# Optimization experiments

Hardware: AMD Instinct MI355X
Metric: run time of the kernel (lower is better)

The kernel has to match this reference:

```python
import jax, jax.numpy as jnp
import numpy as np

W_RAD = 2  # box-filter radius (init kwarg w)
KSIZE = 2 * W_RAD + 1


def _box_conv3d(x, kernel):
    # x: [B,1,D,H,W], kernel: [1,1,k,k,k]; 'same' padding, stride 1
    return jax.lax.conv_general_dilated(
        x, kernel,
        window_strides=(1, 1, 1),
        padding=[(W_RAD, W_RAD)] * 3,
        dimension_numbers=("NCDHW", "OIDHW", "NCDHW"),
    )


def setup_inputs() -> dict:
    key = jax.random.key(0)
    k1, k2 = jax.random.split(key)
    shape = (2, 1, 160, 160, 160)
    M = jax.random.uniform(k1, shape, dtype=jnp.float32)
    R = jax.random.uniform(k2, shape, dtype=jnp.float32)
    kernel = jnp.ones((1, 1, KSIZE, KSIZE, KSIZE), dtype=jnp.float32) / (KSIZE ** 3)
    return {"M": M, "R": R, "kernel": kernel}


def reference(M, R, kernel):
    M_m = _box_conv3d(M, kernel)
    R_m = _box_conv3d(R, kernel)
    MM_m = _box_conv3d(M * M, kernel)
    RR_m = _box_conv3d(R * R, kernel)
    MR_m = _box_conv3d(M * R, kernel)
    M_var = jnp.sqrt(MM_m - M_m ** 2 + 1e-05)
    R_var = jnp.sqrt(RR_m - R_m ** 2 + 1e-05)
    corr = (MR_m - M_m * R_m) / (M_var * R_var + 1e-05)
    return -jnp.mean(corr)
```

## Files before the change

kernel.cpp:

```cpp
#include <hip/hip_runtime.h>
#include <math.h>

#define Dd 160
#define Hh 160
#define Ww 160
#define TW 32
#define TH 32
#define DCHUNK 16
#define NSLICE (DCHUNK + 4)
#define NT 320
#define NCH 5
#define PDIM 36
#define SLICE (Hh * Ww)
#define NDC (Dd / DCHUNK)

__global__ void lncc_zero(float* out) { out[0] = 0.0f; }

__device__ __forceinline__ void bar_lgkm() {
    asm volatile("s_waitcnt lgkmcnt(0)" ::: "memory");
    __builtin_amdgcn_s_barrier();
    asm volatile("" ::: "memory");
}

__global__ __launch_bounds__(NT, 2)
void lncc_main(const float* __restrict__ M, const float* __restrict__ R,
               const float* __restrict__ kern, float* __restrict__ out)
{
    __shared__ float sw[2][NCH][TW][PDIM];
    __shared__ float red[NT / 64];

    const int tid = threadIdx.x;
    const int w0 = blockIdx.x * TW;
    const int h0 = blockIdx.y * TH;
    const int b  = blockIdx.z / NDC;
    const int d0 = (blockIdx.z % NDC) * DCHUNK;
    const float k0 = kern[0];

    const bool isB = tid < (TH + 4) * 8;
    const int g   = tid & 7;
    const int row = tid >> 3;
    const int gh  = h0 + row - 2;
    const bool hok = isB && gh >= 0 && gh < Hh;
    bool qok[3]; int qoff[3];
#pragma unroll
    for (int k = 0; k < 3; ++k) {
        int gw = w0 - 4 + 4 * (g + k);
        qok[k]  = hok && gw >= 0 && gw <= Ww - 4;
        qoff[k] = gh * Ww + gw;
    }
    const size_t bb = (size_t)b * Dd * SLICE;
    const float* Mb = M + bb;
    const float* Rb = R + bb;

    float4 cm[2][3], cr[2][3];

    auto issue = [&](int s, int pp) {
        int dd = d0 - 2 + s;
        bool dok = dd >= 0 && dd < Dd;
        const float* Ms = Mb + (size_t)(dok ? dd : 0) * SLICE;
        const float* Rs = Rb + (size_t)(dok ? dd : 0) * SLICE;
#pragma unroll
        for (int k = 0; k < 3; ++k) {
            bool ok = dok && qok[k];
            cm[pp][k] = ok ? *(const float4*)(Ms + qoff[k]) : make_float4(0.f, 0.f, 0.f, 0.f);
            cr[pp][k] = ok ? *(const float4*)(Rs + qoff[k]) : make_float4(0.f, 0.f, 0.f, 0.f);
        }
    };

    auto bphase = [&](int sp) {
        if (!isB) return;
        float am[12], ar[12];
        *(float4*)&am[0] = cm[sp][0]; *(float4*)&am[4] = cm[sp][1]; *(float4*)&am[8] = cm[sp][2];
        *(float4*)&ar[0] = cr[sp][0]; *(float4*)&ar[4] = cr[sp][1]; *(float4*)&ar[8] = cr[sp][2];
        float mm[8], rr[8], mr[8];
#pragma unroll
        for (int k2 = 0; k2 < 8; ++k2) {
            float a = am[k2 + 2], r_ = ar[k2 + 2];
            mm[k2] = a * a; rr[k2] = r_ * r_; mr[k2] = a * r_;
        }
        float sm  = am[2] + am[3] + am[4] + am[5] + am[6];
        float sr_ = ar[2] + ar[3] + ar[4] + ar[5] + ar[6];
        float smm = mm[0] + mm[1] + mm[2] + mm[3] + mm[4];
        float srr = rr[0] + rr[1] + rr[2] + rr[3] + rr[4];
        float smr = mr[0] + mr[1] + mr[2] + mr[3] + mr[4];
#pragma unroll
        for (int j = 0; j < 4; ++j) {
            if (j) {
                sm  += am[j + 6] - am[j + 1];
                sr_ += ar[j + 6] - ar[j + 1];
                smm += mm[j + 4] - mm[j - 1];
                srr += rr[j + 4] - rr[j - 1];
                smr += mr[j + 4] - mr[j - 1];
            }
            const int wq = 4 * g + j;
            sw[sp][0][wq][row] = sm;
            sw[sp][1][wq][row] = sr_;
            sw[sp][2][wq][row] = smm;
            sw[sp][3][wq][row] = srr;
            sw[sp][4][wq][row] = smr;
        }
    };

    const bool isC = tid < 256;
    const int cw = tid & 31;
    const int hg = (tid >> 5) & 7;

    float S[NCH][4];
    float ring[5][NCH][4];
#pragma unroll
    for (int c = 0; c < NCH; ++c)
#pragma unroll
        for (int j = 0; j < 4; ++j) {
            S[c][j] = 0.f;
#pragma unroll
            for (int t = 0; t < 5; ++t) ring[t][c][j] = 0.f;
        }
    float acc = 0.f;

    auto cphase = [&](int cs, int cp, int slot) {
        if (!isC) return;
        const float* base = &sw[cp][0][cw][hg * 4];
        float4 A  = *(const float4*)(base);
        float4 Bq = *(const float4*)(base + 4);
#pragma unroll
        for (int c = 0; c < NCH; ++c) {
            float4 An, Bn;
            if (c < 4) {
                An = *(const float4*)(base + (c + 1) * TW * PDIM);
                Bn = *(const float4*)(base + (c + 1) * TW * PDIM + 4);
            }
            float t0 = A.x + A.y + A.z + A.w + Bq.x;
            float t1 = t0 + Bq.y - A.x;
            float t2 = t1 + Bq.z - A.y;
            float t3 = t2 + Bq.w - A.z;
            S[c][0] += t0 - ring[slot][c][0]; ring[slot][c][0] = t0;
            S[c][1] += t1 - ring[slot][c][1]; ring[slot][c][1] = t1;
            S[c][2] += t2 - ring[slot][c][2]; ring[slot][c][2] = t2;
            S[c][3] += t3 - ring[slot][c][3]; ring[slot][c][3] = t3;
            A = An; Bq = Bn;
        }
        if (cs >= 4) {
#pragma unroll
            for (int j = 0; j < 4; ++j) {
                float Mm  = S[0][j] * k0, Rm = S[1][j] * k0;
                float MMm = S[2][j] * k0, RRm = S[3][j] * k0, MRm = S[4][j] * k0;
                float Mv = sqrtf(MMm - Mm * Mm + 1e-5f);
                float Rv = sqrtf(RRm - Rm * Rm + 1e-5f);
                acc += (MRm - Mm * Rm) / (Mv * Rv + 1e-5f);
            }
        }
    };

    issue(0, 0);
    issue(1, 1);
    bphase(0);
    issue(2, 0);

    for (int m = 0; m < 2; ++m) {
#pragma unroll
        for (int k = 0; k < 10; ++k) {
            const int s  = m * 10 + k + 1;
            const int sp = (k + 1) & 1;
            const int cp = k & 1;
            const int sl = k % 5;
            bar_lgkm();
            if (s <= NSLICE - 1) {
                bphase(sp);
                if (s + 2 <= NSLICE - 1) issue(s + 2, sp);
            }
            cphase(s - 1, cp, sl);
        }
    }

#pragma unroll
    for (int off = 32; off; off >>= 1) acc += __shfl_down(acc, off, 64);
    if ((tid & 63) == 0) red[tid >> 6] = acc;
    __syncthreads();
    if (tid == 0) {
        float t = red[0] + red[1] + red[2] + red[3] + red[4];
        atomicAdd(out, -t * (1.0f / 8192000.0f));
    }
}

extern "C" void kernel_launch(void* const* d_in, const int* in_sizes, int n_in,
                              void* d_out, int out_size, void* d_ws, size_t ws_size,
                              hipStream_t stream) {
    const float* M = (const float*)d_in[0];
    const float* R = (const float*)d_in[1];
    const float* K = (const float*)d_in[2];
    float* out = (float*)d_out;

    lncc_zero<<<1, 1, 0, stream>>>(out);

    dim3 grid(Ww / TW, Hh / TH, 2 * NDC);
    lncc_main<<<grid, NT, 0, stream>>>(M, R, K, out);
}
```

Baseline: 141.9 us.

## Split warps into dedicated load/box and column-sum roles with smaller tiles

Threads are split into 256 producer threads that load and do W-direction sums and 256 consumer threads that do the H/D sums, in 512-thread blocks. Tiles shrink to 28 rows in H (6 tiles with bounds checks) and 10 slices in D, which raises the block count and targets 4 blocks per CU. The running depth sum S is dropped and recomputed from the 5-slot ring each output slice, cutting register pressure at the cost of a few more adds. The smaller D chunk raises the relative halo reload overhead, and the thread remapping changes the shared-memory access pattern.

```diff
diff --git a/kernel.cpp b/kernel.cpp
--- a/kernel.cpp
+++ b/kernel.cpp
@@ -5,14 +5,16 @@
 #define Hh 160
 #define Ww 160
 #define TW 32
-#define TH 32
-#define DCHUNK 16
+#define TH 28
+#define NHT 6
+#define DCHUNK 10
 #define NSLICE (DCHUNK + 4)
-#define NT 320
+#define NDC (Dd / DCHUNK)
+#define NT 512
 #define NCH 5
+#define HR 32
 #define PDIM 36
 #define SLICE (Hh * Ww)
-#define NDC (Dd / DCHUNK)
 
 __global__ void lncc_zero(float* out) { out[0] = 0.0f; }
 
@@ -22,7 +24,7 @@
     asm volatile("" ::: "memory");
 }
 
-__global__ __launch_bounds__(NT, 2)
+__global__ __launch_bounds__(NT, 4)
 void lncc_main(const float* __restrict__ M, const float* __restrict__ R,
                const float* __restrict__ kern, float* __restrict__ out)
 {
@@ -32,13 +34,16 @@
     const int tid = threadIdx.x;
     const int w0 = blockIdx.x * TW;
     const int h0 = blockIdx.y * TH;
-    const int b  = blockIdx.z / NDC;
-    const int d0 = (blockIdx.z % NDC) * DCHUNK;
+    const int b  = blockIdx.z >> 4;
+    const int d0 = (blockIdx.z & 15) * DCHUNK;
     const float k0 = kern[0];
 
-    const bool isB = tid < (TH + 4) * 8;
-    const int g   = tid & 7;
-    const int row = tid >> 3;
+    const bool isB = tid >= 256;
+    const bool isC = tid < 256;
+
+    const int bt  = tid - 256;
+    const int row = (bt & 15) | ((bt & 64) >> 2);
+    const int g   = ((bt >> 4) & 3) | ((bt & 128) >> 5);
     const int gh  = h0 + row - 2;
     const bool hok = isB && gh >= 0 && gh < Hh;
     bool qok[3]; int qoff[3];
@@ -53,8 +58,8 @@
     const float* Rb = R + bb;
 
     float4 cm[2][3], cr[2][3];
-
     auto issue = [&](int s, int pp) {
+        if (!isB) return;
         int dd = d0 - 2 + s;
         bool dok = dd >= 0 && dd < Dd;
         const float* Ms = Mb + (size_t)(dok ? dd : 0) * SLICE;
@@ -101,75 +106,64 @@
         }
     };
 
-    const bool isC = tid < 256;
     const int cw = tid & 31;
-    const int hg = (tid >> 5) & 7;
+    const int hg = tid >> 5;
+    const bool cact = isC && hg < 7;
 
-    float S[NCH][4];
     float ring[5][NCH][4];
 #pragma unroll
-    for (int c = 0; c < NCH; ++c)
+    for (int t = 0; t < 5; ++t)
 #pragma unroll
-        for (int j = 0; j < 4; ++j) {
-            S[c][j] = 0.f;
+        for (int c = 0; c < NCH; ++c)
 #pragma unroll
-            for (int t = 0; t < 5; ++t) ring[t][c][j] = 0.f;
-        }
+            for (int j = 0; j < 4; ++j) ring[t][c][j] = 0.f;
     float acc = 0.f;
 
     auto cphase = [&](int cs, int cp, int slot) {
-        if (!isC) return;
-        const float* base = &sw[cp][0][cw][hg * 4];
-        float4 A  = *(const float4*)(base);
-        float4 Bq = *(const float4*)(base + 4);
+        if (!cact) return;
+        const float* base = &sw[cp][0][cw][4 * hg];
 #pragma unroll
         for (int c = 0; c < NCH; ++c) {
-            float4 An, Bn;
-            if (c < 4) {
-                An = *(const float4*)(base + (c + 1) * TW * PDIM);
-                Bn = *(const float4*)(base + (c + 1) * TW * PDIM + 4);
-            }
+            float4 A  = *(const float4*)(base + c * TW * PDIM);
+            float4 Bq = *(const float4*)(base + c * TW * PDIM + 4);
             float t0 = A.x + A.y + A.z + A.w + Bq.x;
             float t1 = t0 + Bq.y - A.x;
             float t2 = t1 + Bq.z - A.y;
             float t3 = t2 + Bq.w - A.z;
-            S[c][0] += t0 - ring[slot][c][0]; ring[slot][c][0] = t0;
-            S[c][1] += t1 - ring[slot][c][1]; ring[slot][c][1] = t1;
-            S[c][2] += t2 - ring[slot][c][2]; ring[slot][c][2] = t2;
-            S[c][3] += t3 - ring[slot][c][3]; ring[slot][c][3] = t3;
-            A = An; Bq = Bn;
+            ring[slot][c][0] = t0;
+            ring[slot][c][1] = t1;
+            ring[slot][c][2] = t2;
+            ring[slot][c][3] = t3;
         }
         if (cs >= 4) {
 #pragma unroll
             for (int j = 0; j < 4; ++j) {
-                float Mm  = S[0][j] * k0, Rm = S[1][j] * k0;
-                float MMm = S[2][j] * k0, RRm = S[3][j] * k0, MRm = S[4][j] * k0;
-                float Mv = sqrtf(MMm - Mm * Mm + 1e-5f);
-                float Rv = sqrtf(RRm - Rm * Rm + 1e-5f);
-                acc += (MRm - Mm * Rm) / (Mv * Rv + 1e-5f);
+                if (h0 + 4 * hg + j < Hh) {
+                    float S[NCH];
+#pragma unroll
+                    for (int c = 0; c < NCH; ++c)
+                        S[c] = ring[0][c][j] + ring[1][c][j] + ring[2][c][j]
+                             + ring[3][c][j] + ring[4][c][j];
+                    float Mm  = S[0] * k0, Rm = S[1] * k0;
+                    float MMm = S[2] * k0, RRm = S[3] * k0, MRm = S[4] * k0;
+                    float Mv = sqrtf(MMm - Mm * Mm + 1e-5f);
+                    float Rv = sqrtf(RRm - Rm * Rm + 1e-5f);
+                    acc += (MRm - Mm * Rm) / (Mv * Rv + 1e-5f);
+                }
             }
         }
     };
 
     issue(0, 0);
     issue(1, 1);
-    bphase(0);
-    issue(2, 0);
-
-    for (int m = 0; m < 2; ++m) {
 #pragma unroll
-        for (int k = 0; k < 10; ++k) {
-            const int s  = m * 10 + k + 1;
-            const int sp = (k + 1) & 1;
-            const int cp = k & 1;
-            const int sl = k % 5;
-            bar_lgkm();
-            if (s <= NSLICE - 1) {
-                bphase(sp);
-                if (s + 2 <= NSLICE - 1) issue(s + 2, sp);
-            }
-            cphase(s - 1, cp, sl);
+    for (int k = 0; k <= NSLICE; ++k) {
+        if (k) bar_lgkm();
+        if (k < NSLICE) {
+            bphase(k & 1);
+            if (k + 2 < NSLICE) issue(k + 2, k & 1);
         }
+        if (k >= 1) cphase(k - 1, (k - 1) & 1, (k - 1) % 5);
     }
 
 #pragma unroll
@@ -177,7 +171,9 @@
     if ((tid & 63) == 0) red[tid >> 6] = acc;
     __syncthreads();
     if (tid == 0) {
-        float t = red[0] + red[1] + red[2] + red[3] + red[4];
+        float t = 0.f;
+#pragma unroll
+        for (int i = 0; i < NT / 64; ++i) t += red[i];
         atomicAdd(out, -t * (1.0f / 8192000.0f));
     }
 }
@@ -192,6 +188,6 @@
 
     lncc_zero<<<1, 1, 0, stream>>>(out);
 
-    dim3 grid(Ww / TW, Hh / TH, 2 * NDC);
+    dim3 grid(Ww / TW, NHT, 2 * NDC);
     lncc_main<<<grid, NT, 0, stream>>>(M, R, K, out);
 }
```

After: 269.5 us. +89.9%, slower.
